# Kernel optimization log

Measured on AMD Instinct MI355X. Metric: run time of the kernel, lower is better.

Reference implementation:

```python
import jax, jax.numpy as jnp
from jax import lax
import numpy as np

T, B, K = 512, 2048, 32
START, END, PAD = K - 3, K - 2, K - 1
NEG = -10000.0


def setup_inputs() -> dict:
    key = jax.random.key(0)
    k1, k2, k3 = jax.random.split(key, 3)
    hiddens = jax.random.normal(k1, (T, B, K), dtype=jnp.float32)
    # masks: 0 for valid steps, 1 for padding at the end of each sequence
    lengths = jax.random.randint(k2, (B,), T // 2, T + 1)  # [B]
    masks = (jnp.arange(T)[:, None] >= lengths[None, :]).astype(jnp.float32)  # [T, B]
    # transition[j, i]: score of moving from tag i to tag j (per torch indexing)
    trans = jax.random.normal(k3, (K, K), dtype=jnp.float32)
    trans = trans.at[START, :].set(NEG)
    trans = trans.at[:, END].set(NEG)
    trans = trans.at[:, PAD].set(NEG)
    trans = trans.at[PAD, :].set(NEG)
    trans = trans.at[PAD, END].set(0.0)
    trans = trans.at[PAD, PAD].set(0.0)
    return {"hiddens": hiddens, "masks": masks, "transition": trans}


def reference(hiddens, masks, transition):
    # hiddens: [T, B, K] emissions, masks: [T, B] (1 = pad), transition: [K, K]
    Kt = transition.shape[0]
    Bt = hiddens.shape[1]
    score0 = jnp.full((Bt, Kt), NEG, dtype=hiddens.dtype).at[:, START].set(0.0)

    def step(score, xm):
        hidden, mask = xm  # [B, K], [B]
        # s[b, j, i] = score[b, i] + hidden[b, j] + transition[j, i]
        s = score[:, None, :] + hidden[:, :, None] + transition[None, :, :]
        new = jax.nn.logsumexp(s, axis=2)  # [B, K]
        m = mask[:, None]
        return new * (1.0 - m) + score * m, None

    score, _ = lax.scan(step, score0, (hiddens, masks))
    return jax.nn.logsumexp(score + transition[END][None, :], axis=1)  # [B]
```

## Files before the change

### kernel.cpp

```cpp
#include <hip/hip_runtime.h>


#define T_LEN 512
#define B_SZ  2048
#define K_SZ  32
#define TBK   (B_SZ * K_SZ)
#define HALF_T 256
#define START_S 29
#define END_S   30
#define L2E 1.4426950408889634f
#define LN2 0.6931471805599453f

#if defined(__has_builtin) && __has_builtin(__builtin_amdgcn_logf)
#define LOG2F(x) __builtin_amdgcn_logf(x)
#else
#define LOG2F(x) log2f(x)
#endif

__device__ __forceinline__ float matvec32(const float* eb, const float (&w)[K_SZ]) {
  float s0 = 0.f, s1 = 0.f, s2 = 0.f, s3 = 0.f;
  #pragma unroll
  for (int q = 0; q < 8; ++q) {
    float4 v = *(const float4*)&eb[q * 4];
    s0 = fmaf(v.x, w[q * 4 + 0], s0);
    s1 = fmaf(v.y, w[q * 4 + 1], s1);
    s2 = fmaf(v.z, w[q * 4 + 2], s2);
    s3 = fmaf(v.w, w[q * 4 + 3], s3);
  }
  return (s0 + s1) + (s2 + s3);
}

__global__ __launch_bounds__(256, 2) void crf_scan(
    const float* __restrict__ hid, const float* __restrict__ msk,
    const float* __restrict__ trans,
    float* __restrict__ EA, float* __restrict__ RA,
    float* __restrict__ EB, float* __restrict__ RB)
{
  __shared__ float eb[8][2][32];

  const int tx   = threadIdx.x;
  const int lane = tx & 31;
  const int grp  = tx >> 5;
  const bool fwd = (blockIdx.x < 256);
  const int  bid = fwd ? blockIdx.x : (blockIdx.x - 256);
  const int  tid = bid * 256 + tx;
  const int  b   = tid >> 5;

  float R = 0.f;

  if (fwd) {
    float w[K_SZ];
    #pragma unroll
    for (int j = 0; j < K_SZ; ++j) w[j] = exp2f(trans[lane * K_SZ + j] * L2E);

    float e = (lane == START_S) ? 1.f : 0.f;
    const float* hp = hid + tid;

    float ehr[8];
    #pragma unroll
    for (int k = 0; k < 8; ++k) ehr[k] = exp2f(hp[k * TBK] * L2E);

    for (int t0 = 0; t0 < HALF_T; t0 += 8) {
      #pragma unroll
      for (int k = 0; k < 8; ++k) {
        float ehc = ehr[k];
        float hn  = hp[(t0 + 8 + k) * TBK];
        eb[grp][k & 1][lane] = e;
        float sum = matvec32(&eb[grp][k & 1][0], w);
        ehr[k] = exp2f(hn * L2E);
        e = sum * ehc;
        if ((k & 3) == 3) {
          float c = __shfl(e, 0, 32);
          int   s = ilogbf(c);
          e = ldexpf(e, -s);
          R += (float)s;
        }
      }
    }
    EA[tid] = e;
    if (lane == 0) RA[b] = R;
  } else {
    float w[K_SZ];
    #pragma unroll
    for (int i = 0; i < K_SZ; ++i) w[i] = exp2f(trans[i * K_SZ + lane] * L2E);

    float e = exp2f(trans[END_S * K_SZ + lane] * L2E);
    const float* hp = hid + (long)(T_LEN - 1) * TBK + tid;
    const float* mp = msk + (long)(T_LEN - 1) * B_SZ + b;

    float ehr[8], mr[8];
    #pragma unroll
    for (int k = 0; k < 8; ++k) {
      ehr[k] = exp2f(hp[-(long)k * TBK] * L2E);
      mr[k]  = mp[-(long)k * B_SZ];
    }

    for (int t0 = 0; t0 < HALF_T; t0 += 8) {
      #pragma unroll
      for (int k = 0; k < 8; ++k) {
        float ehc = ehr[k];
        float mv  = mr[k];
        long  nx  = t0 + 8 + k; nx = (nx <= HALF_T - 1) ? nx : (HALF_T - 1);
        float hn  = hp[-nx * TBK];
        float mn  = mp[-nx * B_SZ];
        float f = e * ehc;
        eb[grp][k & 1][lane] = f;
        float sum = matvec32(&eb[grp][k & 1][0], w);
        ehr[k] = exp2f(hn * L2E);
        mr[k]  = mn;
        e = (mv > 0.5f) ? e : sum;
        if ((k & 3) == 3) {
          float c = __shfl(e, 0, 32);
          int   s = ilogbf(c);
          e = ldexpf(e, -s);
          R += (float)s;
        }
      }
    }
    EB[tid] = e;
    if (lane == 0) RB[b] = R;
  }
}

__global__ __launch_bounds__(256) void crf_combine(
    const float* __restrict__ EA, const float* __restrict__ RA,
    const float* __restrict__ EB, const float* __restrict__ RB,
    float* __restrict__ out)
{
  const int tid  = blockIdx.x * 256 + threadIdx.x;
  const int lane = tid & 31;
  const int b    = tid >> 5;

  float la = LOG2F(EA[tid]);
  float lb = LOG2F(EB[tid]);
  float v  = la + lb;
  float M  = v;
  M = fmaxf(M, __shfl_xor(M, 1));
  M = fmaxf(M, __shfl_xor(M, 2));
  M = fmaxf(M, __shfl_xor(M, 4));
  M = fmaxf(M, __shfl_xor(M, 8));
  M = fmaxf(M, __shfl_xor(M, 16));
  float x = exp2f(v - M);
  x += __shfl_xor(x, 1);
  x += __shfl_xor(x, 2);
  x += __shfl_xor(x, 4);
  x += __shfl_xor(x, 8);
  x += __shfl_xor(x, 16);
  if (lane == 0) out[b] = (RA[b] + RB[b] + M + LOG2F(x)) * LN2;
}

extern "C" void kernel_launch(void* const* d_in, const int* in_sizes, int n_in,
                              void* d_out, int out_size, void* d_ws, size_t ws_size,
                              hipStream_t stream) {
  const float* hid   = (const float*)d_in[0];
  const float* msk   = (const float*)d_in[1];
  const float* trans = (const float*)d_in[2];
  float* out = (float*)d_out;

  float* W  = (float*)d_ws;
  float* EA = W;
  float* RA = W + TBK;
  float* EB = W + TBK + B_SZ;
  float* RB = W + TBK + B_SZ + TBK;

  crf_scan<<<dim3(512), dim3(256), 0, stream>>>(hid, msk, trans, EA, RA, EB, RB);
  crf_combine<<<dim3(TBK / 256), dim3(256), 0, stream>>>(EA, RA, EB, RB, out);
}
```

Measured before the change: 221.6 us.

## Batch 32 sequences per wave and do CRF transition matvec with bf16 MFMA

The per-thread scalar matvec through shared memory is replaced. Each 64-lane wave now handles 32 batch elements at once, and each time step becomes two 32x32x16 bf16 MFMA instructions against the exponentiated transition matrix. The state is converted to bf16 B-operands with cvt_pk and permlane32_swap. Emission loads become float4 prefetches kept DEPTH steps ahead, and renormalization uses an integer exponent extracted from the float bits. This cuts the instruction count and LDS traffic of the serial forward/backward recurrences, at the cost of bf16 rounding of the state and transition weights and far fewer waves (128) in flight.

```diff
diff --git a/kernel.cpp b/kernel.cpp
--- a/kernel.cpp
+++ b/kernel.cpp
@@ -4,149 +4,208 @@
 #define T_LEN 512
 #define B_SZ  2048
 #define K_SZ  32
-#define TBK   (B_SZ * K_SZ)
-#define HALF_T 256
+#define TBK   65536
 #define START_S 29
 #define END_S   30
 #define L2E 1.4426950408889634f
 #define LN2 0.6931471805599453f
-
+#define DEPTH 4
+
+#if defined(__has_builtin) && __has_builtin(__builtin_amdgcn_exp2f)
+#define EXP2F(x) __builtin_amdgcn_exp2f(x)
+#else
+#define EXP2F(x) exp2f(x)
+#endif
 #if defined(__has_builtin) && __has_builtin(__builtin_amdgcn_logf)
 #define LOG2F(x) __builtin_amdgcn_logf(x)
 #else
 #define LOG2F(x) log2f(x)
 #endif
 
-__device__ __forceinline__ float matvec32(const float* eb, const float (&w)[K_SZ]) {
-  float s0 = 0.f, s1 = 0.f, s2 = 0.f, s3 = 0.f;
-  #pragma unroll
-  for (int q = 0; q < 8; ++q) {
-    float4 v = *(const float4*)&eb[q * 4];
-    s0 = fmaf(v.x, w[q * 4 + 0], s0);
-    s1 = fmaf(v.y, w[q * 4 + 1], s1);
-    s2 = fmaf(v.z, w[q * 4 + 2], s2);
-    s3 = fmaf(v.w, w[q * 4 + 3], s3);
-  }
-  return (s0 + s1) + (s2 + s3);
-}
-
-__global__ __launch_bounds__(256, 2) void crf_scan(
+typedef float f32x16 __attribute__((ext_vector_type(16)));
+typedef short s16x8  __attribute__((ext_vector_type(8)));
+
+static __device__ __forceinline__ unsigned cvtpk(float lo, float hi) {
+  unsigned r;
+  asm("v_cvt_pk_bf16_f32 %0, %1, %2" : "=v"(r) : "v"(lo), "v"(hi));
+  return r;
+}
+static __device__ __forceinline__ void swap32(unsigned &a, unsigned &b) {
+  asm("v_permlane32_swap_b32 %0, %1" : "+v"(a), "+v"(b));
+}
+static __device__ __forceinline__ s16x8 pack8(unsigned a0, unsigned a1, unsigned a2, unsigned a3) {
+  union { unsigned u[4]; s16x8 v; } t;
+  t.u[0] = a0; t.u[1] = a1; t.u[2] = a2; t.u[3] = a3;
+  return t.v;
+}
+
+static __device__ __forceinline__ void toB(const f32x16& d, s16x8& B1, s16x8& B2) {
+  unsigned c0 = cvtpk(d[0],  d[1]),  c1 = cvtpk(d[2],  d[3]);
+  unsigned c2 = cvtpk(d[4],  d[5]),  c3 = cvtpk(d[6],  d[7]);
+  swap32(c0, c2); swap32(c1, c3);
+  B1 = pack8(c0, c1, c2, c3);
+  unsigned e0 = cvtpk(d[8],  d[9]),  e1 = cvtpk(d[10], d[11]);
+  unsigned e2 = cvtpk(d[12], d[13]), e3 = cvtpk(d[14], d[15]);
+  swap32(e0, e2); swap32(e1, e3);
+  B2 = pack8(e0, e1, e2, e3);
+}
+
+template<int FWD>
+static __device__ __forceinline__ void scan_body(
     const float* __restrict__ hid, const float* __restrict__ msk,
     const float* __restrict__ trans,
-    float* __restrict__ EA, float* __restrict__ RA,
-    float* __restrict__ EB, float* __restrict__ RB)
+    float* __restrict__ E_out, int* __restrict__ R_out, int g)
 {
-  __shared__ float eb[8][2][32];
-
-  const int tx   = threadIdx.x;
-  const int lane = tx & 31;
-  const int grp  = tx >> 5;
-  const bool fwd = (blockIdx.x < 256);
-  const int  bid = fwd ? blockIdx.x : (blockIdx.x - 256);
-  const int  tid = bid * 256 + tx;
-  const int  b   = tid >> 5;
-
-  float R = 0.f;
-
-  if (fwd) {
-    float w[K_SZ];
+  const int l   = threadIdx.x & 63;
+  const int col = l & 31;
+  const int h2  = l >> 5;
+  const int b   = g * K_SZ + col;
+
+  s16x8 A1, A2;
+  {
+    float v[16];
     #pragma unroll
-    for (int j = 0; j < K_SZ; ++j) w[j] = exp2f(trans[lane * K_SZ + j] * L2E);
-
-    float e = (lane == START_S) ? 1.f : 0.f;
-    const float* hp = hid + tid;
-
-    float ehr[8];
+    for (int jj = 0; jj < 8; ++jj) {
+      const int k1 = 8 * h2 + jj, k2 = 16 + 8 * h2 + jj;
+      v[jj]     = FWD ? trans[col * K_SZ + k1] : trans[k1 * K_SZ + col];
+      v[8 + jj] = FWD ? trans[col * K_SZ + k2] : trans[k2 * K_SZ + col];
+    }
+    A1 = pack8(cvtpk(EXP2F(v[0] * L2E),  EXP2F(v[1] * L2E)),
+               cvtpk(EXP2F(v[2] * L2E),  EXP2F(v[3] * L2E)),
+               cvtpk(EXP2F(v[4] * L2E),  EXP2F(v[5] * L2E)),
+               cvtpk(EXP2F(v[6] * L2E),  EXP2F(v[7] * L2E)));
+    A2 = pack8(cvtpk(EXP2F(v[8]  * L2E), EXP2F(v[9]  * L2E)),
+               cvtpk(EXP2F(v[10] * L2E), EXP2F(v[11] * L2E)),
+               cvtpk(EXP2F(v[12] * L2E), EXP2F(v[13] * L2E)),
+               cvtpk(EXP2F(v[14] * L2E), EXP2F(v[15] * L2E)));
+  }
+
+  f32x16 d, dini;
+  #pragma unroll
+  for (int r = 0; r < 16; ++r) {
+    const int row = (r & 3) + 8 * (r >> 2) + 4 * h2;
+    if (FWD) { d[r] = (row == START_S) ? 1.0f : 0.0f; dini[r] = 0.0f; }
+    else     { dini[r] = EXP2F(trans[END_S * K_SZ + row] * L2E); d[r] = dini[r]; }
+  }
+
+  const long hstep = FWD ? (long)TBK : -(long)TBK;
+  const long mstep = FWD ? (long)B_SZ : -(long)B_SZ;
+  const float* hp = hid + (FWD ? 0 : (long)(T_LEN - 1) * TBK) + (long)b * K_SZ + 4 * h2;
+  const float* mp = msk + (FWD ? 0 : (long)(T_LEN - 1) * B_SZ) + b;
+
+  float4 hr[DEPTH][4];
+  float  mr[DEPTH];
+  #pragma unroll
+  for (int k = 0; k < DEPTH; ++k) {
+    const float* p = hp + (long)k * hstep;
+    hr[k][0] = *(const float4*)(p);
+    hr[k][1] = *(const float4*)(p + 8);
+    hr[k][2] = *(const float4*)(p + 16);
+    hr[k][3] = *(const float4*)(p + 24);
+    mr[k] = FWD ? 0.0f : mp[(long)k * mstep];
+  }
+
+  int R = 0;
+  for (int c = 0; c < 64; ++c) {
     #pragma unroll
-    for (int k = 0; k < 8; ++k) ehr[k] = exp2f(hp[k * TBK] * L2E);
-
-    for (int t0 = 0; t0 < HALF_T; t0 += 8) {
-      #pragma unroll
-      for (int k = 0; k < 8; ++k) {
-        float ehc = ehr[k];
-        float hn  = hp[(t0 + 8 + k) * TBK];
-        eb[grp][k & 1][lane] = e;
-        float sum = matvec32(&eb[grp][k & 1][0], w);
-        ehr[k] = exp2f(hn * L2E);
-        e = sum * ehc;
-        if ((k & 3) == 3) {
-          float c = __shfl(e, 0, 32);
-          int   s = ilogbf(c);
-          e = ldexpf(e, -s);
-          R += (float)s;
-        }
+    for (int k = 0; k < DEPTH; ++k) {
+      const float4 e0 = hr[k][0], e1 = hr[k][1], e2 = hr[k][2], e3 = hr[k][3];
+      const float  mv = FWD ? 0.0f : mr[k];
+      {
+        const float* p = hp + (long)(c * DEPTH + k + DEPTH) * hstep;
+        hr[k][0] = *(const float4*)(p);
+        hr[k][1] = *(const float4*)(p + 8);
+        hr[k][2] = *(const float4*)(p + 16);
+        hr[k][3] = *(const float4*)(p + 24);
+        if (!FWD) mr[k] = mp[(long)(c * DEPTH + k + DEPTH) * mstep];
+      }
+      f32x16 eh;
+      eh[0]  = EXP2F(e0.x * L2E); eh[1]  = EXP2F(e0.y * L2E);
+      eh[2]  = EXP2F(e0.z * L2E); eh[3]  = EXP2F(e0.w * L2E);
+      eh[4]  = EXP2F(e1.x * L2E); eh[5]  = EXP2F(e1.y * L2E);
+      eh[6]  = EXP2F(e1.z * L2E); eh[7]  = EXP2F(e1.w * L2E);
+      eh[8]  = EXP2F(e2.x * L2E); eh[9]  = EXP2F(e2.y * L2E);
+      eh[10] = EXP2F(e2.z * L2E); eh[11] = EXP2F(e2.w * L2E);
+      eh[12] = EXP2F(e3.x * L2E); eh[13] = EXP2F(e3.y * L2E);
+      eh[14] = EXP2F(e3.z * L2E); eh[15] = EXP2F(e3.w * L2E);
+
+      if (FWD) {
+        s16x8 B1, B2; toB(d, B1, B2);
+        f32x16 z = {0.0f};
+        d = __builtin_amdgcn_mfma_f32_32x32x16_bf16(A1, B1, z, 0, 0, 0);
+        d = __builtin_amdgcn_mfma_f32_32x32x16_bf16(A2, B2, d, 0, 0, 0);
+        #pragma unroll
+        for (int r = 0; r < 16; ++r) d[r] *= eh[r];
+      } else {
+        #pragma unroll
+        for (int r = 0; r < 16; ++r) d[r] *= eh[r];
+        s16x8 B1, B2; toB(d, B1, B2);
+        f32x16 z = {0.0f};
+        f32x16 dn = __builtin_amdgcn_mfma_f32_32x32x16_bf16(A1, B1, z, 0, 0, 0);
+        dn = __builtin_amdgcn_mfma_f32_32x32x16_bf16(A2, B2, dn, 0, 0, 0);
+        const bool m = mv > 0.5f;
+        #pragma unroll
+        for (int r = 0; r < 16; ++r) d[r] = m ? dini[r] : dn[r];
+      }
+
+      if (k == DEPTH - 1) {
+        const float c0 = __shfl(d[0], col);
+        const unsigned bb = __float_as_uint(c0);
+        int   s  = (int)((bb >> 23) & 255) - 127;
+        float sc = __uint_as_float((unsigned)(127 - s) << 23);
+        if (!FWD) { const bool m = mv > 0.5f; sc = m ? 1.0f : sc; s = m ? 0 : s; }
+        #pragma unroll
+        for (int r = 0; r < 16; ++r) d[r] *= sc;
+        R += s;
       }
     }
-    EA[tid] = e;
-    if (lane == 0) RA[b] = R;
-  } else {
-    float w[K_SZ];
-    #pragma unroll
-    for (int i = 0; i < K_SZ; ++i) w[i] = exp2f(trans[i * K_SZ + lane] * L2E);
-
-    float e = exp2f(trans[END_S * K_SZ + lane] * L2E);
-    const float* hp = hid + (long)(T_LEN - 1) * TBK + tid;
-    const float* mp = msk + (long)(T_LEN - 1) * B_SZ + b;
-
-    float ehr[8], mr[8];
-    #pragma unroll
-    for (int k = 0; k < 8; ++k) {
-      ehr[k] = exp2f(hp[-(long)k * TBK] * L2E);
-      mr[k]  = mp[-(long)k * B_SZ];
-    }
-
-    for (int t0 = 0; t0 < HALF_T; t0 += 8) {
-      #pragma unroll
-      for (int k = 0; k < 8; ++k) {
-        float ehc = ehr[k];
-        float mv  = mr[k];
-        long  nx  = t0 + 8 + k; nx = (nx <= HALF_T - 1) ? nx : (HALF_T - 1);
-        float hn  = hp[-nx * TBK];
-        float mn  = mp[-nx * B_SZ];
-        float f = e * ehc;
-        eb[grp][k & 1][lane] = f;
-        float sum = matvec32(&eb[grp][k & 1][0], w);
-        ehr[k] = exp2f(hn * L2E);
-        mr[k]  = mn;
-        e = (mv > 0.5f) ? e : sum;
-        if ((k & 3) == 3) {
-          float c = __shfl(e, 0, 32);
-          int   s = ilogbf(c);
-          e = ldexpf(e, -s);
-          R += (float)s;
-        }
-      }
-    }
-    EB[tid] = e;
-    if (lane == 0) RB[b] = R;
-  }
-}
-
-__global__ __launch_bounds__(256) void crf_combine(
-    const float* __restrict__ EA, const float* __restrict__ RA,
-    const float* __restrict__ EB, const float* __restrict__ RB,
+  }
+
+  float* eo = E_out + (long)b * K_SZ + 4 * h2;
+  #pragma unroll
+  for (int q = 0; q < 4; ++q) {
+    float4 o = { d[4 * q + 0], d[4 * q + 1], d[4 * q + 2], d[4 * q + 3] };
+    *(float4*)(eo + 8 * q) = o;
+  }
+  if (h2 == 0) R_out[b] = R;
+}
+
+__global__ __launch_bounds__(64, 1) void crf_scan(
+    const float* __restrict__ hid, const float* __restrict__ msk,
+    const float* __restrict__ trans,
+    float* __restrict__ EA, int* __restrict__ RA,
+    float* __restrict__ EB, int* __restrict__ RB)
+{
+  const int bid = blockIdx.x;
+  if (bid < 64) scan_body<1>(hid, msk, trans, EA, RA, bid);
+  else          scan_body<0>(hid, msk, trans, EB, RB, bid - 64);
+}
+
+__global__ __launch_bounds__(256) void crf_comb(
+    const float* __restrict__ EA, const int* __restrict__ RA,
+    const float* __restrict__ EB, const int* __restrict__ RB,
     float* __restrict__ out)
 {
-  const int tid  = blockIdx.x * 256 + threadIdx.x;
-  const int lane = tid & 31;
-  const int b    = tid >> 5;
-
-  float la = LOG2F(EA[tid]);
-  float lb = LOG2F(EB[tid]);
-  float v  = la + lb;
-  float M  = v;
+  const int tx = threadIdx.x;
+  const int i  = tx & 31;
+  const int g  = tx >> 5;
+  const int b  = blockIdx.x * 8 + g;
+
+  const float va = EA[b * K_SZ + i], vb = EB[b * K_SZ + i];
+  float v = LOG2F(va) + LOG2F(vb);
+  float M = v;
   M = fmaxf(M, __shfl_xor(M, 1));
   M = fmaxf(M, __shfl_xor(M, 2));
   M = fmaxf(M, __shfl_xor(M, 4));
   M = fmaxf(M, __shfl_xor(M, 8));
   M = fmaxf(M, __shfl_xor(M, 16));
-  float x = exp2f(v - M);
+  float x = EXP2F(v - M);
   x += __shfl_xor(x, 1);
   x += __shfl_xor(x, 2);
   x += __shfl_xor(x, 4);
   x += __shfl_xor(x, 8);
   x += __shfl_xor(x, 16);
-  if (lane == 0) out[b] = (RA[b] + RB[b] + M + LOG2F(x)) * LN2;
+  if (i == 0) out[b] = ((float)(RA[b] + RB[b]) + M + LOG2F(x)) * LN2;
 }
 
 extern "C" void kernel_launch(void* const* d_in, const int* in_sizes, int n_in,
@@ -157,12 +216,11 @@
   const float* trans = (const float*)d_in[2];
   float* out = (float*)d_out;
 
-  float* W  = (float*)d_ws;
-  float* EA = W;
-  float* RA = W + TBK;
-  float* EB = W + TBK + B_SZ;
-  float* RB = W + TBK + B_SZ + TBK;
-
-  crf_scan<<<dim3(512), dim3(256), 0, stream>>>(hid, msk, trans, EA, RA, EB, RB);
-  crf_combine<<<dim3(TBK / 256), dim3(256), 0, stream>>>(EA, RA, EB, RB, out);
-}
+  float* EA = (float*)d_ws;
+  float* EB = EA + (size_t)B_SZ * K_SZ;
+  int*   RA = (int*)(EB + (size_t)B_SZ * K_SZ);
+  int*   RB = RA + B_SZ;
+
+  crf_scan<<<dim3(128), dim3(64), 0, stream>>>(hid, msk, trans, EA, RA, EB, RB);
+  crf_comb<<<dim3(B_SZ / 8), dim3(256), 0, stream>>>(EA, RA, EB, RB, out);
+}
```

Measured after the change: 325.0 us. 46.6% more time.
